# Kernel optimization log

Hardware: AMD Instinct MI355X
Metric: run time of the kernel (lower is better)

Reference implementation:

```python
import jax, jax.numpy as jnp
import numpy as np

N_NODES = 100000
N_EDGES = 1600000
HIDDEN = 64
FILTERS = 64
GAUSS = 5
SHORT = 5
N_CONV = 2
Z_DIM = 2 * FILTERS + SHORT  # CGConv concat [x_i, x_j, e]


def setup_inputs() -> dict:
    key = jax.random.key(0)
    ks = jax.random.split(key, 12)
    h = jax.random.normal(ks[0], (N_NODES, HIDDEN), dtype=jnp.float32)
    edge_index = jax.random.randint(ks[1], (2, N_EDGES), 0, N_NODES, dtype=jnp.int64)
    edge_weight = jax.random.uniform(ks[2], (N_EDGES,), dtype=jnp.float32)
    edge_attr = jax.random.uniform(ks[3], (N_EDGES, GAUSS), dtype=jnp.float32)
    s = 1.0 / np.sqrt(HIDDEN)
    lin0_w = jax.random.uniform(ks[4], (HIDDEN, FILTERS), jnp.float32, -s, s)
    lin0_b = jax.random.uniform(ks[5], (FILTERS,), jnp.float32, -s, s)
    s2 = 1.0 / np.sqrt(GAUSS)
    short_w = jax.random.uniform(ks[6], (GAUSS, SHORT), jnp.float32, -s2, s2)
    short_b = jax.random.uniform(ks[7], (SHORT,), jnp.float32, -s2, s2)
    s3 = 1.0 / np.sqrt(Z_DIM)
    conv_f_w = jax.random.uniform(ks[8], (N_CONV, Z_DIM, FILTERS), jnp.float32, -s3, s3)
    conv_f_b = jax.random.uniform(ks[9], (N_CONV, FILTERS), jnp.float32, -s3, s3)
    conv_s_w = jax.random.uniform(ks[10], (N_CONV, Z_DIM, FILTERS), jnp.float32, -s3, s3)
    conv_s_b = jax.random.uniform(ks[11], (N_CONV, FILTERS), jnp.float32, -s3, s3)
    return {
        'h': h, 'edge_index': edge_index, 'edge_weight': edge_weight,
        'edge_attr': edge_attr, 'data': 0,
        'lin0_w': lin0_w, 'lin0_b': lin0_b,
        'short_w': short_w, 'short_b': short_b,
        'conv_f_w': conv_f_w, 'conv_f_b': conv_f_b,
        'conv_s_w': conv_s_w, 'conv_s_b': conv_s_b,
    }


def _cgconv(x, src, dst, e, wf, bf, ws, bs):
    # z = [x_i, x_j, e]; split the matmul to avoid materializing z[E, 2F+5]
    x_i = x[dst]  # target node features [E, F]
    x_j = x[src]  # source node features [E, F]
    F_ = x.shape[1]
    zf = x_i @ wf[:F_] + x_j @ wf[F_:2 * F_] + e @ wf[2 * F_:] + bf
    zs = x_i @ ws[:F_] + x_j @ ws[F_:2 * F_] + e @ ws[2 * F_:] + bs
    msg = jax.nn.sigmoid(zf) * jax.nn.softplus(zs)  # gated messages [E, F]
    agg = jax.ops.segment_sum(msg, dst, num_segments=x.shape[0])
    return x + agg  # residual, aggr='add', batch_norm=False


def reference(h, edge_index, edge_weight, edge_attr, data,
              lin0_w, lin0_b, short_w, short_b,
              conv_f_w, conv_f_b, conv_s_w, conv_s_b):
    out = jax.nn.relu(h @ lin0_w + lin0_b)          # [N, F]
    e = jax.nn.relu(edge_attr @ short_w + short_b)  # [E, 5]
    src, dst = edge_index[0], edge_index[1]
    for i in range(N_CONV):
        out = jax.nn.relu(_cgconv(out, src, dst, e,
                                  conv_f_w[i], conv_f_b[i],
                                  conv_s_w[i], conv_s_b[i]))
    return out
```

## Files before the change

kernel.cpp:

```cpp
#include <hip/hip_runtime.h>

#define NN 100000
#define NE 1600000
#define NSB 391

#define LOG2E 1.4426950408889634f
#define LN2 0.6931471805599453f

typedef short short4v __attribute__((ext_vector_type(4)));
typedef short short8v __attribute__((ext_vector_type(8)));
typedef float f32x2 __attribute__((ext_vector_type(2)));
typedef float f32x4 __attribute__((ext_vector_type(4)));
typedef unsigned u32x4 __attribute__((ext_vector_type(4)));

static __device__ __forceinline__ unsigned f2bf(float x) {
    unsigned b = __float_as_uint(x);
    return (b + 0x7FFFu + ((b >> 16) & 1u)) >> 16;
}
static __device__ __forceinline__ float bflo(unsigned u) { return __uint_as_float(u << 16); }
static __device__ __forceinline__ float bfhi(unsigned u) { return __uint_as_float(u & 0xFFFF0000u); }
static __device__ __forceinline__ int imin(int a, int b) { return a < b ? a : b; }
static __device__ __forceinline__ short8v mk8(short4v a, short4v b) {
    short8v r;
    r[0] = a[0]; r[1] = a[1]; r[2] = a[2]; r[3] = a[3];
    r[4] = b[0]; r[5] = b[1]; r[6] = b[2]; r[7] = b[3];
    return r;
}

static __device__ __forceinline__ float edge_acc(uint4 m, unsigned ps, f32x2 pd2,
                                                 const f32x2* __restrict__ w2, float acc) {
    f32x2 z;
    z.x = bflo(ps);
    z.y = bfhi(ps);
    z += pd2;
    const float e50 = bflo(m.y), e51 = bfhi(m.y);
    const float e52 = bflo(m.z), e53 = bfhi(m.z);
    const float e54 = bflo(m.w);
    z += e50 * w2[0];
    z += e51 * w2[1];
    z += e52 * w2[2];
    z += e53 * w2[3];
    z += e54 * w2[4];
    const float sig = __builtin_amdgcn_rcpf(1.f + __builtin_amdgcn_exp2f(z.x));
    const float gg = fmaxf(z.y, 0.f) +
                     __builtin_amdgcn_logf(1.f + __builtin_amdgcn_exp2f(-fabsf(z.y)));
    return fmaf(sig, gg, acc);
}

__global__ __launch_bounds__(256) void k_wpack(const float* __restrict__ cfw,
                                               const float* __restrict__ csw,
                                               const float* __restrict__ l0w,
                                               unsigned short* __restrict__ Bp) {
    const int qq = blockIdx.x * 256 + threadIdx.x;
    const float* src;
    float scale;
    int roff, ct, kh, l;
    if (qq < 4096) {
        const int layer = qq >> 11;
        const int q = qq & 2047;
        const int m = q >> 9;
        const int rem = q & 511;
        ct = rem >> 7;
        kh = (rem >> 6) & 1;
        l = rem & 63;
        scale = (m & 1) ? LOG2E : -LOG2E;
        src = ((m & 1) ? csw : cfw) + (size_t)layer * 133 * 64;
        roff = (m >> 1) ? 64 : 0;
    } else {
        const int p = qq - 4096;
        ct = p >> 7;
        kh = (p >> 6) & 1;
        l = p & 63;
        scale = 1.f;
        src = l0w;
        roff = 0;
    }
    const int n = ct * 16 + (l & 15);
#pragma unroll
    for (int j = 0; j < 8; j++) {
        const int k = kh * 32 + ((j < 4) ? (4 * (l >> 4) + j) : (16 + 4 * (l >> 4) + j - 4));
        Bp[(size_t)qq * 8 + j] = (unsigned short)f2bf(scale * src[(size_t)(roff + k) * 64 + n]);
    }
}

__global__ __launch_bounds__(256) void k_lin0m_hist(const float* __restrict__ h,
                                                    const unsigned short* __restrict__ Bp0,
                                                    const float* __restrict__ b,
                                                    float* __restrict__ x0,
                                                    unsigned short* __restrict__ xb,
                                                    const int* __restrict__ ei,
                                                    int* __restrict__ cnt,
                                                    int* __restrict__ rank) {
    __shared__ __align__(16) short xl[32 * 64];
    if (blockIdx.x < 1250) {
        const int base = blockIdx.x * 1280 + threadIdx.x;
        int r[5];
#pragma unroll
        for (int j = 0; j < 5; j++) r[j] = atomicAdd(&cnt[ei[NE + base + j * 256]], 1);
#pragma unroll
        for (int j = 0; j < 5; j++) rank[base + j * 256] = r[j];
        return;
    }
    const int rowbase = (blockIdx.x - 1250) * 32;
    {
        const float4* hs = (const float4*)(h + (size_t)rowbase * 64);
#pragma unroll
        for (int it = 0; it < 2; it++) {
            const float4 v = hs[threadIdx.x + it * 256];
            short4v sv;
            sv[0] = (short)f2bf(v.x);
            sv[1] = (short)f2bf(v.y);
            sv[2] = (short)f2bf(v.z);
            sv[3] = (short)f2bf(v.w);
            *(short4v*)&xl[(threadIdx.x + it * 256) * 4] = sv;
        }
    }
    __syncthreads();
    const int ct = threadIdx.x >> 6;
    const int l = threadIdx.x & 63;
    const int lm = l & 15;
    const int g = l >> 4;
    short8v A[2][2];
#pragma unroll
    for (int rt = 0; rt < 2; rt++) {
        const short* xrow = &xl[(rt * 16 + lm) * 64];
        A[rt][0] = mk8(*(const short4v*)&xrow[g * 4], *(const short4v*)&xrow[16 + g * 4]);
        A[rt][1] = mk8(*(const short4v*)&xrow[32 + g * 4], *(const short4v*)&xrow[48 + g * 4]);
    }
    const short* bp = (const short*)Bp0;
    const short8v B0 = *(const short8v*)&bp[((ct * 2 + 0) * 64 + l) * 8];
    const short8v B1 = *(const short8v*)&bp[((ct * 2 + 1) * 64 + l) * 8];
    const int col = ct * 16 + lm;
    const float bc = b[col];
#pragma unroll
    for (int rt = 0; rt < 2; rt++) {
        f32x4 a = {0.f, 0.f, 0.f, 0.f};
        a = __builtin_amdgcn_mfma_f32_16x16x32_bf16(A[rt][0], B0, a, 0, 0, 0);
        a = __builtin_amdgcn_mfma_f32_16x16x32_bf16(A[rt][1], B1, a, 0, 0, 0);
#pragma unroll
        for (int reg = 0; reg < 4; reg++) {
            const int rowg = rowbase + rt * 16 + g * 4 + reg;
            const float r = fmaxf(a[reg] + bc, 0.f);
            x0[(size_t)rowg * 64 + col] = r;
            xb[(size_t)rowg * 64 + col] = (unsigned short)f2bf(r);
        }
    }
}

__global__ __launch_bounds__(256) void k_scan1(const int* __restrict__ cnt,
                                               int* __restrict__ offs, int* __restrict__ bsum) {
    __shared__ int sm[256];
    const int t = threadIdx.x;
    const int i = blockIdx.x * 256 + t;
    const int v = (i < NN) ? cnt[i] : 0;
    sm[t] = v;
    __syncthreads();
    for (int off = 1; off < 256; off <<= 1) {
        const int x = (t >= off) ? sm[t - off] : 0;
        __syncthreads();
        sm[t] += x;
        __syncthreads();
    }
    if (i < NN) offs[i] = sm[t] - v;
    if (t == 255) bsum[blockIdx.x] = sm[255];
}

__global__ __launch_bounds__(512) void k_scan2(int* __restrict__ bsum) {
    __shared__ int sm[512];
    const int t = threadIdx.x;
    const int v = (t < NSB) ? bsum[t] : 0;
    sm[t] = v;
    __syncthreads();
    for (int off = 1; off < 512; off <<= 1) {
        const int x = (t >= off) ? sm[t - off] : 0;
        __syncthreads();
        sm[t] += x;
        __syncthreads();
    }
    if (t < NSB) bsum[t] = sm[t] - v;
}

__global__ __launch_bounds__(256) void k_scan3(int* __restrict__ offs,
                                               const int* __restrict__ bsum) {
    const int i = blockIdx.x * 256 + threadIdx.x;
    if (i < NN) offs[i] += bsum[blockIdx.x];
    if (i == 0) offs[NN] = NE;
}

__global__ __launch_bounds__(256) void k_scat_proj(const int* __restrict__ ei,
                                                   const float* __restrict__ eattr,
                                                   const float* __restrict__ sw,
                                                   const float* __restrict__ sb,
                                                   const int* __restrict__ rank,
                                                   const int* __restrict__ offs,
                                                   unsigned* __restrict__ meta,
                                                   const unsigned short* __restrict__ xb,
                                                   const unsigned short* __restrict__ Bp,
                                                   const float* __restrict__ bfv,
                                                   const float* __restrict__ bsv,
                                                   unsigned* __restrict__ Pd,
                                                   unsigned* __restrict__ Ps) {
    __shared__ __align__(16) short xl[32 * 64];
    if (blockIdx.x < 1250) {
        __shared__ float swl[25], sbl[5];
        if (threadIdx.x < 25) swl[threadIdx.x] = sw[threadIdx.x];
        if (threadIdx.x >= 32 && threadIdx.x < 37) sbl[threadIdx.x - 32] = sb[threadIdx.x - 32];
        __syncthreads();
        const int base = blockIdx.x * 1280 + threadIdx.x;
        int s[5], d[5], r[5];
        float ea[5][5];
#pragma unroll
        for (int j = 0; j < 5; j++) {
            const int e = base + j * 256;
            s[j] = ei[e];
            d[j] = ei[NE + e];
            r[j] = rank[e];
#pragma unroll
            for (int k = 0; k < 5; k++) ea[j][k] = eattr[(size_t)e * 5 + k];
        }
        int pos[5];
#pragma unroll
        for (int j = 0; j < 5; j++) pos[j] = offs[d[j]] + r[j];
#pragma unroll
        for (int j = 0; j < 5; j++) {
            unsigned u5[5];
#pragma unroll
            for (int k = 0; k < 5; k++) {
                float a = sbl[k];
#pragma unroll
                for (int q = 0; q < 5; q++) a += ea[j][q] * swl[q * 5 + k];
                u5[k] = f2bf(fmaxf(a, 0.f));
            }
            u32x4 m;
            m[0] = (unsigned)s[j];
            m[1] = u5[0] | (u5[1] << 16);
            m[2] = u5[2] | (u5[3] << 16);
            m[3] = u5[4];
            __builtin_nontemporal_store(m, (u32x4*)&meta[(size_t)pos[j] * 4]);
        }
        return;
    }
    const int rowbase = (blockIdx.x - 1250) * 32;
    {
        const u32x4* xsrc = (const u32x4*)(xb + (size_t)rowbase * 64);
        u32x4* xdst = (u32x4*)xl;
        xdst[threadIdx.x] = __builtin_nontemporal_load(&xsrc[threadIdx.x]);
    }
    __syncthreads();
    const int ct = threadIdx.x >> 6;
    const int l = threadIdx.x & 63;
    const int lm = l & 15;
    const int g = l >> 4;
    short8v A[2][2];
#pragma unroll
    for (int rt = 0; rt < 2; rt++) {
        const short* xrow = &xl[(rt * 16 + lm) * 64];
        A[rt][0] = mk8(*(const short4v*)&xrow[g * 4], *(const short4v*)&xrow[16 + g * 4]);
        A[rt][1] = mk8(*(const short4v*)&xrow[32 + g * 4], *(const short4v*)&xrow[48 + g * 4]);
    }
    const short* bp = (const short*)Bp;
    f32x4 acc[4][2];
#pragma unroll
    for (int m = 0; m < 4; m++) {
        const short8v B0 = *(const short8v*)&bp[(((m * 4 + ct) * 2 + 0) * 64 + l) * 8];
        const short8v B1 = *(const short8v*)&bp[(((m * 4 + ct) * 2 + 1) * 64 + l) * 8];
#pragma unroll
        for (int rt = 0; rt < 2; rt++) {
            f32x4 a = {0.f, 0.f, 0.f, 0.f};
            a = __builtin_amdgcn_mfma_f32_16x16x32_bf16(A[rt][0], B0, a, 0, 0, 0);
            a = __builtin_amdgcn_mfma_f32_16x16x32_bf16(A[rt][1], B1, a, 0, 0, 0);
            acc[m][rt] = a;
        }
    }
    const int col = ct * 16 + lm;
    const float bfb = -LOG2E * bfv[col];
    const float bsb = LOG2E * bsv[col];
#pragma unroll
    for (int rt = 0; rt < 2; rt++) {
#pragma unroll
        for (int reg = 0; reg < 4; reg++) {
            const int rowg = rowbase + rt * 16 + g * 4 + reg;
            Pd[(size_t)rowg * 64 + col] =
                f2bf(acc[0][rt][reg] + bfb) | (f2bf(acc[1][rt][reg] + bsb) << 16);
            Ps[(size_t)rowg * 64 + col] =
                f2bf(acc[2][rt][reg]) | (f2bf(acc[3][rt][reg]) << 16);
        }
    }
}

__global__ __launch_bounds__(256) void k_projm(const unsigned short* __restrict__ xb,
                                               const unsigned short* __restrict__ Bp,
                                               const float* __restrict__ bfv,
                                               const float* __restrict__ bsv,
                                               unsigned* __restrict__ Pd,
                                               unsigned* __restrict__ Ps) {
    __shared__ __align__(16) short xl[32 * 64];
    const int rowbase = blockIdx.x * 32;
    {
        const u32x4* xsrc = (const u32x4*)(xb + (size_t)rowbase * 64);
        u32x4* xdst = (u32x4*)xl;
        xdst[threadIdx.x] = __builtin_nontemporal_load(&xsrc[threadIdx.x]);
    }
    __syncthreads();
    const int ct = threadIdx.x >> 6;
    const int l = threadIdx.x & 63;
    const int lm = l & 15;
    const int g = l >> 4;
    short8v A[2][2];
#pragma unroll
    for (int rt = 0; rt < 2; rt++) {
        const short* xrow = &xl[(rt * 16 + lm) * 64];
        A[rt][0] = mk8(*(const short4v*)&xrow[g * 4], *(const short4v*)&xrow[16 + g * 4]);
        A[rt][1] = mk8(*(const short4v*)&xrow[32 + g * 4], *(const short4v*)&xrow[48 + g * 4]);
    }
    const short* bp = (const short*)Bp;
    f32x4 acc[4][2];
#pragma unroll
    for (int m = 0; m < 4; m++) {
        const short8v B0 = *(const short8v*)&bp[(((m * 4 + ct) * 2 + 0) * 64 + l) * 8];
        const short8v B1 = *(const short8v*)&bp[(((m * 4 + ct) * 2 + 1) * 64 + l) * 8];
#pragma unroll
        for (int rt = 0; rt < 2; rt++) {
            f32x4 a = {0.f, 0.f, 0.f, 0.f};
            a = __builtin_amdgcn_mfma_f32_16x16x32_bf16(A[rt][0], B0, a, 0, 0, 0);
            a = __builtin_amdgcn_mfma_f32_16x16x32_bf16(A[rt][1], B1, a, 0, 0, 0);
            acc[m][rt] = a;
        }
    }
    const int col = ct * 16 + lm;
    const float bfb = -LOG2E * bfv[col];
    const float bsb = LOG2E * bsv[col];
#pragma unroll
    for (int rt = 0; rt < 2; rt++) {
#pragma unroll
        for (int reg = 0; reg < 4; reg++) {
            const int rowg = rowbase + rt * 16 + g * 4 + reg;
            Pd[(size_t)rowg * 64 + col] =
                f2bf(acc[0][rt][reg] + bfb) | (f2bf(acc[1][rt][reg] + bsb) << 16);
            Ps[(size_t)rowg * 64 + col] =
                f2bf(acc[2][rt][reg]) | (f2bf(acc[3][rt][reg]) << 16);
        }
    }
}

__global__ __launch_bounds__(64) void k_seg(const int* __restrict__ offs,
                                            const uint4* __restrict__ meta,
                                            const unsigned* __restrict__ Pd,
                                            const unsigned* __restrict__ Ps,
                                            const float* __restrict__ wfE,
                                            const float* __restrict__ wsE,
                                            const float* __restrict__ xin,
                                            float* __restrict__ out,
                                            unsigned short* __restrict__ xbout) {
    const int n = blockIdx.x;
    const int lane = threadIdx.x;
    const int start = __builtin_amdgcn_readfirstlane(offs[n]);
    const int end = __builtin_amdgcn_readfirstlane(offs[n + 1]);
    const unsigned pd = __builtin_nontemporal_load(&Pd[(size_t)n * 64 + lane]);
    f32x2 pd2;
    pd2.x = bflo(pd);
    pd2.y = bfhi(pd);
    f32x2 w2[5];
#pragma unroll
    for (int k = 0; k < 5; k++) {
        f32x2 p;
        p.x = -LOG2E * wfE[k * 64 + lane];
        p.y = LOG2E * wsE[k * 64 + lane];
        w2[k] = p;
    }
    const float xv = __builtin_nontemporal_load(&xin[(size_t)n * 64 + lane]);
    float acc = 0.f;
    const int cnt = end - start;
    if (cnt > 0) {
        const int last = end - 1;
        const int nbF = (cnt + 3) >> 2;
        uint4 M0[4], M1[4];
        unsigned PS0[4];
#pragma unroll
        for (int j = 0; j < 4; j++) M0[j] = meta[imin(start + j, last)];
#pragma unroll
        for (int j = 0; j < 4; j++) M1[j] = meta[imin(start + 4 + j, last)];
#pragma unroll
        for (int j = 0; j < 4; j++) PS0[j] = Ps[(size_t)M0[j].x * 64 + lane];
        for (int b = 0; b < nbF - 1; b++) {
            const int base2 = __builtin_amdgcn_readfirstlane(start + (b + 2) * 4);
            uint4 M2[4];
            unsigned PS1[4];
#pragma unroll
            for (int j = 0; j < 4; j++) M2[j] = meta[imin(base2 + j, last)];
#pragma unroll
            for (int j = 0; j < 4; j++) PS1[j] = Ps[(size_t)M1[j].x * 64 + lane];
#pragma unroll
            for (int j = 0; j < 4; j++) acc = edge_acc(M0[j], PS0[j], pd2, w2, acc);
#pragma unroll
            for (int j = 0; j < 4; j++) {
                M0[j] = M1[j];
                M1[j] = M2[j];
                PS0[j] = PS1[j];
            }
        }
        const int lb = start + (nbF - 1) * 4;
#pragma unroll
        for (int j = 0; j < 4; j++)
            if (lb + j < end) acc = edge_acc(M0[j], PS0[j], pd2, w2, acc);
    }
    const float res = fmaxf(fmaf(acc, LN2, xv), 0.f);
    if (xbout) {
        out[(size_t)n * 64 + lane] = res;
        xbout[(size_t)n * 64 + lane] = (unsigned short)f2bf(res);
    } else {
        __builtin_nontemporal_store(res, &out[(size_t)n * 64 + lane]);
    }
}

extern "C" void kernel_launch(void* const* d_in, const int* in_sizes, int n_in,
                              void* d_out, int out_size, void* d_ws, size_t ws_size,
                              hipStream_t stream) {
    const float* h = (const float*)d_in[0];
    const int* ei = (const int*)d_in[1];
    const float* eattr = (const float*)d_in[3];
    const float* lin0_w = (const float*)d_in[5];
    const float* lin0_b = (const float*)d_in[6];
    const float* short_w = (const float*)d_in[7];
    const float* short_b = (const float*)d_in[8];
    const float* conv_f_w = (const float*)d_in[9];
    const float* conv_f_b = (const float*)d_in[10];
    const float* conv_s_w = (const float*)d_in[11];
    const float* conv_s_b = (const float*)d_in[12];

    char* ws = (char*)d_ws;
    uint4* meta = (uint4*)ws;
    float* X0 = (float*)(ws + (size_t)NE * 16);
    float* X1 = X0 + (size_t)NN * 64;
    unsigned* Pd = (unsigned*)(X1 + (size_t)NN * 64);
    unsigned* Ps = Pd + (size_t)NN * 64;
    unsigned short* XB = (unsigned short*)(Ps + (size_t)NN * 64);
    unsigned short* Bp = XB + (size_t)NN * 64;
    int* cnt = (int*)(Bp + 36864);
    int* offs = cnt + NN;
    int* bsum = offs + NN + 1;
    int* rank = (int*)X1;

    hipMemsetAsync(cnt, 0, (size_t)NN * 4, stream);
    k_wpack<<<18, 256, 0, stream>>>(conv_f_w, conv_s_w, lin0_w, Bp);
    k_lin0m_hist<<<1250 + 3125, 256, 0, stream>>>(h, Bp + 32768, lin0_b, X0, XB, ei, cnt, rank);
    k_scan1<<<NSB, 256, 0, stream>>>(cnt, offs, bsum);
    k_scan2<<<1, 512, 0, stream>>>(bsum);
    k_scan3<<<NSB, 256, 0, stream>>>(offs, bsum);
    k_scat_proj<<<1250 + 3125, 256, 0, stream>>>(ei, eattr, short_w, short_b, rank, offs,
                                                 (unsigned*)meta, XB, Bp, conv_f_b, conv_s_b,
                                                 Pd, Ps);
    k_seg<<<NN, 64, 0, stream>>>(offs, meta, Pd, Ps,
                                 conv_f_w + 128 * 64, conv_s_w + 128 * 64,
                                 X0, X1, XB);
    k_projm<<<NN / 32, 256, 0, stream>>>(XB, Bp + 16384, conv_f_b + 64, conv_s_b + 64, Pd, Ps);
    k_seg<<<NN, 64, 0, stream>>>(offs, meta, Pd, Ps,
                                 conv_f_w + 133 * 64 + 128 * 64,
                                 conv_s_w + 133 * 64 + 128 * 64,
                                 X1, (float*)d_out, (unsigned short*)nullptr);
}
```

Baseline: 338.0 us.

## Swizzle LDS tiles for MFMA fragment reads and interleave edge/node blocks

Stores the 32x64 bf16 staging tiles in LDS with an XOR swizzle on 16-byte column blocks and adds a matching fragment-read helper, to cut LDS bank conflicts when building MFMA A operands. Separately, the two fused kernels now interleave edge-work blocks and node-matmul blocks in a 2:5 pattern instead of running all edge blocks first, so atomic/scatter traffic and compute-heavy blocks are in flight together. The swizzle adds some index arithmetic, and the interleaving changes block scheduling order.

```diff
diff --git a/kernel.cpp b/kernel.cpp
--- a/kernel.cpp
+++ b/kernel.cpp
@@ -25,6 +25,22 @@
     r[0] = a[0]; r[1] = a[1]; r[2] = a[2]; r[3] = a[3];
     r[4] = b[0]; r[5] = b[1]; r[6] = b[2]; r[7] = b[3];
     return r;
+}
+
+static __device__ __forceinline__ int swz(int row, int colblk) {
+    return row * 64 + ((colblk ^ (row & 7)) << 3);
+}
+
+static __device__ __forceinline__ void frag_reads(const short* xl, int row, int g,
+                                                  short8v& a0, short8v& a1) {
+    const int sub = (g & 1) * 4;
+    const int cb = g >> 1;
+    const short4v p0 = *(const short4v*)&xl[swz(row, cb + 0) + sub];
+    const short4v p1 = *(const short4v*)&xl[swz(row, cb + 2) + sub];
+    const short4v p2 = *(const short4v*)&xl[swz(row, cb + 4) + sub];
+    const short4v p3 = *(const short4v*)&xl[swz(row, cb + 6) + sub];
+    a0 = mk8(p0, p1);
+    a1 = mk8(p2, p3);
 }
 
 static __device__ __forceinline__ float edge_acc(uint4 m, unsigned ps, f32x2 pd2,
@@ -92,8 +108,10 @@
                                                     int* __restrict__ cnt,
                                                     int* __restrict__ rank) {
     __shared__ __align__(16) short xl[32 * 64];
-    if (blockIdx.x < 1250) {
-        const int base = blockIdx.x * 1280 + threadIdx.x;
+    const int r7 = blockIdx.x % 7;
+    const int q7 = blockIdx.x / 7;
+    if (r7 < 2) {
+        const int base = (q7 * 2 + r7) * 1280 + threadIdx.x;
         int r[5];
 #pragma unroll
         for (int j = 0; j < 5; j++) r[j] = atomicAdd(&cnt[ei[NE + base + j * 256]], 1);
@@ -101,18 +119,20 @@
         for (int j = 0; j < 5; j++) rank[base + j * 256] = r[j];
         return;
     }
-    const int rowbase = (blockIdx.x - 1250) * 32;
+    const int rowbase = (q7 * 5 + (r7 - 2)) * 32;
     {
         const float4* hs = (const float4*)(h + (size_t)rowbase * 64);
 #pragma unroll
         for (int it = 0; it < 2; it++) {
-            const float4 v = hs[threadIdx.x + it * 256];
+            const int i = threadIdx.x + it * 256;
+            const float4 v = hs[i];
             short4v sv;
             sv[0] = (short)f2bf(v.x);
             sv[1] = (short)f2bf(v.y);
             sv[2] = (short)f2bf(v.z);
             sv[3] = (short)f2bf(v.w);
-            *(short4v*)&xl[(threadIdx.x + it * 256) * 4] = sv;
+            const int row = i >> 4;
+            *(short4v*)&xl[swz(row, (i >> 1) & 7) + (i & 1) * 4] = sv;
         }
     }
     __syncthreads();
@@ -122,11 +142,7 @@
     const int g = l >> 4;
     short8v A[2][2];
 #pragma unroll
-    for (int rt = 0; rt < 2; rt++) {
-        const short* xrow = &xl[(rt * 16 + lm) * 64];
-        A[rt][0] = mk8(*(const short4v*)&xrow[g * 4], *(const short4v*)&xrow[16 + g * 4]);
-        A[rt][1] = mk8(*(const short4v*)&xrow[32 + g * 4], *(const short4v*)&xrow[48 + g * 4]);
-    }
+    for (int rt = 0; rt < 2; rt++) frag_reads(xl, rt * 16 + lm, g, A[rt][0], A[rt][1]);
     const short* bp = (const short*)Bp0;
     const short8v B0 = *(const short8v*)&bp[((ct * 2 + 0) * 64 + l) * 8];
     const short8v B1 = *(const short8v*)&bp[((ct * 2 + 1) * 64 + l) * 8];
@@ -201,12 +217,14 @@
                                                    unsigned* __restrict__ Pd,
                                                    unsigned* __restrict__ Ps) {
     __shared__ __align__(16) short xl[32 * 64];
-    if (blockIdx.x < 1250) {
+    const int r7 = blockIdx.x % 7;
+    const int q7 = blockIdx.x / 7;
+    if (r7 < 2) {
         __shared__ float swl[25], sbl[5];
         if (threadIdx.x < 25) swl[threadIdx.x] = sw[threadIdx.x];
         if (threadIdx.x >= 32 && threadIdx.x < 37) sbl[threadIdx.x - 32] = sb[threadIdx.x - 32];
         __syncthreads();
-        const int base = blockIdx.x * 1280 + threadIdx.x;
+        const int base = (q7 * 2 + r7) * 1280 + threadIdx.x;
         int s[5], d[5], r[5];
         float ea[5][5];
 #pragma unroll
@@ -240,11 +258,12 @@
         }
         return;
     }
-    const int rowbase = (blockIdx.x - 1250) * 32;
+    const int rowbase = (q7 * 5 + (r7 - 2)) * 32;
     {
         const u32x4* xsrc = (const u32x4*)(xb + (size_t)rowbase * 64);
-        u32x4* xdst = (u32x4*)xl;
-        xdst[threadIdx.x] = __builtin_nontemporal_load(&xsrc[threadIdx.x]);
+        const int i = threadIdx.x;
+        const u32x4 v = __builtin_nontemporal_load(&xsrc[i]);
+        *(u32x4*)&xl[swz(i >> 3, i & 7)] = v;
     }
     __syncthreads();
     const int ct = threadIdx.x >> 6;
@@ -253,11 +272,7 @@
     const int g = l >> 4;
     short8v A[2][2];
 #pragma unroll
-    for (int rt = 0; rt < 2; rt++) {
-        const short* xrow = &xl[(rt * 16 + lm) * 64];
-        A[rt][0] = mk8(*(const short4v*)&xrow[g * 4], *(const short4v*)&xrow[16 + g * 4]);
-        A[rt][1] = mk8(*(const short4v*)&xrow[32 + g * 4], *(const short4v*)&xrow[48 + g * 4]);
-    }
+    for (int rt = 0; rt < 2; rt++) frag_reads(xl, rt * 16 + lm, g, A[rt][0], A[rt][1]);
     const short* bp = (const short*)Bp;
     f32x4 acc[4][2];
 #pragma unroll
@@ -298,8 +313,9 @@
     const int rowbase = blockIdx.x * 32;
     {
         const u32x4* xsrc = (const u32x4*)(xb + (size_t)rowbase * 64);
-        u32x4* xdst = (u32x4*)xl;
-        xdst[threadIdx.x] = __builtin_nontemporal_load(&xsrc[threadIdx.x]);
+        const int i = threadIdx.x;
+        const u32x4 v = __builtin_nontemporal_load(&xsrc[i]);
+        *(u32x4*)&xl[swz(i >> 3, i & 7)] = v;
     }
     __syncthreads();
     const int ct = threadIdx.x >> 6;
@@ -308,11 +324,7 @@
     const int g = l >> 4;
     short8v A[2][2];
 #pragma unroll
-    for (int rt = 0; rt < 2; rt++) {
-        const short* xrow = &xl[(rt * 16 + lm) * 64];
-        A[rt][0] = mk8(*(const short4v*)&xrow[g * 4], *(const short4v*)&xrow[16 + g * 4]);
-        A[rt][1] = mk8(*(const short4v*)&xrow[32 + g * 4], *(const short4v*)&xrow[48 + g * 4]);
-    }
+    for (int rt = 0; rt < 2; rt++) frag_reads(xl, rt * 16 + lm, g, A[rt][0], A[rt][1]);
     const short* bp = (const short*)Bp;
     f32x4 acc[4][2];
 #pragma unroll
@@ -443,13 +455,13 @@
 
     hipMemsetAsync(cnt, 0, (size_t)NN * 4, stream);
     k_wpack<<<18, 256, 0, stream>>>(conv_f_w, conv_s_w, lin0_w, Bp);
-    k_lin0m_hist<<<1250 + 3125, 256, 0, stream>>>(h, Bp + 32768, lin0_b, X0, XB, ei, cnt, rank);
+    k_lin0m_hist<<<4375, 256, 0, stream>>>(h, Bp + 32768, lin0_b, X0, XB, ei, cnt, rank);
     k_scan1<<<NSB, 256, 0, stream>>>(cnt, offs, bsum);
     k_scan2<<<1, 512, 0, stream>>>(bsum);
     k_scan3<<<NSB, 256, 0, stream>>>(offs, bsum);
-    k_scat_proj<<<1250 + 3125, 256, 0, stream>>>(ei, eattr, short_w, short_b, rank, offs,
-                                                 (unsigned*)meta, XB, Bp, conv_f_b, conv_s_b,
-                                                 Pd, Ps);
+    k_scat_proj<<<4375, 256, 0, stream>>>(ei, eattr, short_w, short_b, rank, offs,
+                                          (unsigned*)meta, XB, Bp, conv_f_b, conv_s_b,
+                                          Pd, Ps);
     k_seg<<<NN, 64, 0, stream>>>(offs, meta, Pd, Ps,
                                  conv_f_w + 128 * 64, conv_s_w + 128 * 64,
                                  X0, X1, XB);
```

Result: no change. 334.5 us (-1.0%).
